# Kernel tuning notes

Measured on AMD Instinct MI355X. Metric: run time of the kernel, lower is better.

## Reference

```python
import jax, jax.numpy as jnp
import numpy as np

K = 256       # num states
M = 2         # markov order
D = 256       # lemb_size
V = 50000     # ntypes (vocab)
T = 512
B = 256
Kp1 = K + 1
EPS = 1e-5
INIT = 0.1


def _layernorm(h, g, b):
    mu = h.mean(-1, keepdims=True)
    var = ((h - mu) ** 2).mean(-1, keepdims=True)
    return (h - mu) / jnp.sqrt(var + EPS) * g + b


def setup_inputs() -> dict:
    key = jax.random.key(0)
    ks = jax.random.split(key, 12)
    u = lambda k, shp: jax.random.uniform(k, shp, jnp.float32, -INIT, INIT)
    return {
        "x": jax.random.randint(ks[0], (T, B), 0, V, dtype=jnp.int32),
        "z": jax.random.randint(ks[1], (T, B), 0, K, dtype=jnp.int32),
        "lembs": u(ks[2], (K, D)),
        "tlembs": u(ks[3], (Kp1, D)),
        "dec_W": u(ks[4], (V, D)),
        "dec_b": jnp.zeros((V,), jnp.float32),
        "em_W": u(ks[5], (D, D)),
        "em_bias": jnp.zeros((D,), jnp.float32),
        "em_g": jnp.ones((D,), jnp.float32),
        "em_beta": jnp.zeros((D,), jnp.float32),
        "td_W": u(ks[6], (K, M * D)),
        "td_b": jnp.zeros((K,), jnp.float32),
        "tm_W": u(ks[7], (M * D, M * D)),
        "tm_bias": jnp.zeros((M * D,), jnp.float32),
        "tn_g": jnp.ones((M * D,), jnp.float32),
        "tn_beta": jnp.zeros((M * D,), jnp.float32),
    }


def reference(x, z, lembs, tlembs, dec_W, dec_b, em_W, em_bias, em_g, em_beta,
              td_W, td_b, tm_W, tm_bias, tn_g, tn_beta):
    # --- emission distribution: K x V log-normalized ---
    h = _layernorm(lembs + jax.nn.relu(lembs @ em_W.T + em_bias), em_g, em_beta)
    emdist = jax.nn.log_softmax(h @ dec_W.T + dec_b, axis=1)  # (K, V)

    # --- transition distribution: (Kp1^M, K) log-normalized ---
    # cartesian product of label embeddings, row-major: row r <-> (i_0,...,i_{M-1})
    idx = jnp.indices((Kp1,) * M).reshape(M, -1)                 # (M, Kp1^M)
    cat = tlembs[idx].transpose(1, 0, 2).reshape(-1, M * D)      # (Kp1^M, M*D)
    th = _layernorm(cat + jax.nn.relu(cat @ tm_W.T + tm_bias), tn_g, tn_beta)
    transdist = jax.nn.log_softmax(th @ td_W.T + td_b, axis=1)   # (Kp1^M, K)

    # --- log_joint ---
    xlps = emdist.T[x]                                           # (T, B, K)
    emlps = jnp.take_along_axis(xlps, z[..., None].astype(jnp.int32), axis=2)[..., 0].sum(0)  # (B,)

    zpad = jnp.concatenate([jnp.full((M, B), K, dtype=z.dtype), z], axis=0)  # (T+M, B)
    win = jnp.stack([zpad[m:m + T] for m in range(M + 1)], 0)    # (M+1, T, B)
    lin = win[0]
    for m in range(1, M):
        lin = lin * Kp1 + win[m]                                 # row index into (Kp1^M, K)
    trans_lps = transdist[lin, win[M]]                           # (T, B)
    return emlps + trans_lps.sum(0)                              # (B,)
```

## Files before the change

kernel.cpp:

```cpp
#include <hip/hip_runtime.h>

#define Kst 256
#define Dd 256
#define Vv 50000
#define VPAD 50176
#define Tt 512
#define Bb 256
#define KP1 257
#define MD 512
#define NROWS (KP1*KP1)
#define EPSf 1e-5f

#define VB2 196
#define VB3 (VB2*4)

typedef __attribute__((ext_vector_type(8))) short short8;
typedef __attribute__((ext_vector_type(4))) float f32x4;
typedef __attribute__((ext_vector_type(4))) unsigned u32x4;
typedef __attribute__((ext_vector_type(2))) unsigned u32x2;

__device__ __forceinline__ unsigned short f2bf(float f) {
    unsigned u = __builtin_bit_cast(unsigned, f);
    unsigned r = (u + 0x7fffu + ((u >> 16) & 1u)) >> 16;
    return (unsigned short)r;
}
__device__ __forceinline__ float bf2f(unsigned short u) {
    return __builtin_bit_cast(float, ((unsigned)u) << 16);
}
__device__ __forceinline__ unsigned bfpack(float lo, float hi) {
    return __builtin_amdgcn_perm(__builtin_bit_cast(unsigned, hi),
                                 __builtin_bit_cast(unsigned, lo), 0x07060302u);
}
__device__ __forceinline__ unsigned f2bf2(float lo, float hi) {
    return (unsigned)f2bf(lo) | ((unsigned)f2bf(hi) << 16);
}

__global__ __launch_bounds__(256) void k_hP(
    const float* __restrict__ lembs, const float* __restrict__ em_W,
    const float* __restrict__ em_bias, const float* __restrict__ em_g,
    const float* __restrict__ em_beta, unsigned short* __restrict__ h_bf,
    const float* __restrict__ tlembs, const float* __restrict__ tm_W,
    float* __restrict__ P0, float* __restrict__ P1,
    const float* __restrict__ td_W, const float* __restrict__ tn_g,
    const float* __restrict__ tn_beta, const float* __restrict__ td_b,
    unsigned short* __restrict__ tdwg_bf, float* __restrict__ Gt,
    float* __restrict__ Bt, const float* __restrict__ dec_W,
    unsigned short* __restrict__ dwP)
{
    int bid = blockIdx.x;
    int tid = threadIdx.x, lane = tid & 63, wv = tid >> 6;
    int l15 = lane & 15, q = lane >> 4;

    if (bid >= 108) {
        int pb = bid - 108;
        int v = pb*8 + wv*2 + (lane >> 5);
        int l32 = lane & 31;
        int vr = v < Vv ? v : Vv-1;
        const float* src = dec_W + (size_t)vr*Dd + l32*8;
        float4 f0 = *(const float4*)(src);
        float4 f1 = *(const float4*)(src + 4);
        u32x4 pk;
        pk.x = bfpack(f0.x, f0.y);
        pk.y = bfpack(f0.z, f0.w);
        pk.z = bfpack(f1.x, f1.y);
        pk.w = bfpack(f1.z, f1.w);
        int ks = l32 >> 2, q2 = l32 & 3;
        int vb2 = v >> 8, vl = v & 255;
        int wvv = vl >> 6, ctv = vl & 3, l15v = (vl >> 2) & 15;
        *(short8*)(dwP + ((((size_t)vb2*8 + ks)*16 + wvv*4 + ctv)*64
                          + (q2*16 + l15v))*8) = __builtin_bit_cast(short8, pk);
        return;
    }

    if (bid >= 44) {
        int c = (bid - 44)*4 + wv;
        const float4* w4 = (const float4*)(td_W + (size_t)c*MD);
        const float4* g4 = (const float4*)tn_g;
        const float4* b4 = (const float4*)tn_beta;
        float sg = 0.f, sb = 0.f;
        short8 o;
        #pragma unroll
        for (int u = 0; u < 2; ++u) {
            int j4 = lane*2 + u;
            float4 w = w4[j4], g = g4[j4], bt = b4[j4];
            sg += w.x*g.x + w.y*g.y + w.z*g.z + w.w*g.w;
            sb += w.x*bt.x + w.y*bt.y + w.z*bt.z + w.w*bt.w;
            o[u*4+0] = (short)f2bf(w.x*g.x);
            o[u*4+1] = (short)f2bf(w.y*g.y);
            o[u*4+2] = (short)f2bf(w.z*g.z);
            o[u*4+3] = (short)f2bf(w.w*g.w);
        }
        {
            int wvv = c >> 6, l15v = (c >> 2) & 15, ctv = c & 3;
            int ksv = lane >> 2, qv = lane & 3;
            *(short8*)(tdwg_bf +
                ((((size_t)wvv*16 + ksv)*4 + ctv)*64 + (qv*16 + l15v))*8) = o;
        }
        #pragma unroll
        for (int dd = 32; dd > 0; dd >>= 1) {
            sg += __shfl_xor(sg, dd);
            sb += __shfl_xor(sb, dd);
        }
        if (lane == 0) { Gt[c] = sg; Bt[c] = sb + td_b[c]; }
        return;
    }

    __shared__ short ta[32][264];
    __shared__ float lsep[4][32][2];
    __shared__ float musig[32][2];

    int job, r0, cb, koff, BK;
    const float* Arow; const float* Brow;
    if (bid < 8) {
        job = 0; r0 = bid*32; cb = 0; koff = 0; BK = Dd;
        Arow = lembs; Brow = em_W;
    } else {
        int b2 = bid - 8;
        int half = b2 / 18;
        int b3 = b2 % 18;
        job = 1 + half;
        r0 = (b3 >> 1) * 32;
        cb = (b3 & 1) * 256;
        koff = half * 256; BK = MD;
        Arow = tlembs; Brow = tm_W;
    }

    {
        int row = tid >> 3, seg = (tid & 7) * 32;
        int r = r0 + row;
        if (r > 256) r = 256;
        const float4* s4 = (const float4*)(Arow + (size_t)r*Dd + seg);
        #pragma unroll
        for (int u = 0; u < 4; ++u) {
            float4 f0 = s4[u*2], f1 = s4[u*2+1];
            u32x4 pk;
            pk.x = bfpack(f0.x, f0.y);
            pk.y = bfpack(f0.z, f0.w);
            pk.z = bfpack(f1.x, f1.y);
            pk.w = bfpack(f1.z, f1.w);
            *(short8*)&ta[row][seg + u*8] = __builtin_bit_cast(short8, pk);
        }
    }
    __syncthreads();

    const float* bptr[4];
    #pragma unroll
    for (int ct = 0; ct < 4; ++ct) {
        int j = cb + wv*64 + ct*16 + l15;
        bptr[ct] = Brow + (size_t)j*BK + koff + q*8;
    }
    f32x4 acc[2][4];
    #pragma unroll
    for (int rt = 0; rt < 2; ++rt)
        #pragma unroll
        for (int ct = 0; ct < 4; ++ct)
            acc[rt][ct] = (f32x4){0.f,0.f,0.f,0.f};
    for (int ks = 0; ks < 8; ++ks) {
        short8 a0 = *(const short8*)&ta[ 0 + l15][ks*32 + q*8];
        short8 a1 = *(const short8*)&ta[16 + l15][ks*32 + q*8];
        short8 b[4];
        #pragma unroll
        for (int ct = 0; ct < 4; ++ct) {
            float4 f0 = *(const float4*)(bptr[ct] + ks*32);
            float4 f1 = *(const float4*)(bptr[ct] + ks*32 + 4);
            u32x4 pk;
            pk.x = bfpack(f0.x, f0.y);
            pk.y = bfpack(f0.z, f0.w);
            pk.z = bfpack(f1.x, f1.y);
            pk.w = bfpack(f1.z, f1.w);
            b[ct] = __builtin_bit_cast(short8, pk);
        }
        #pragma unroll
        for (int ct = 0; ct < 4; ++ct) {
            acc[0][ct] = __builtin_amdgcn_mfma_f32_16x16x32_bf16(a0, b[ct], acc[0][ct], 0,0,0);
            acc[1][ct] = __builtin_amdgcn_mfma_f32_16x16x32_bf16(a1, b[ct], acc[1][ct], 0,0,0);
        }
    }

    if (job != 0) {
        float* Pd = (job == 1) ? P0 : P1;
        #pragma unroll
        for (int rt = 0; rt < 2; ++rt) {
            #pragma unroll
            for (int reg = 0; reg < 4; ++reg) {
                int r = r0 + rt*16 + q*4 + reg;
                if (r < KP1) {
                    float* dst = Pd + (size_t)r*MD + cb + wv*64;
                    #pragma unroll
                    for (int ct = 0; ct < 4; ++ct)
                        dst[ct*16 + l15] = acc[rt][ct][reg];
                }
            }
        }
        return;
    }

    float bias_c[4];
    #pragma unroll
    for (int ct = 0; ct < 4; ++ct)
        bias_c[ct] = em_bias[wv*64 + ct*16 + l15];
    #pragma unroll
    for (int rt = 0; rt < 2; ++rt) {
        #pragma unroll
        for (int reg = 0; reg < 4; ++reg) {
            int r = r0 + rt*16 + q*4 + reg;
            #pragma unroll
            for (int ct = 0; ct < 4; ++ct) {
                float lv = lembs[(size_t)r*Dd + wv*64 + ct*16 + l15];
                acc[rt][ct][reg] = lv + fmaxf(acc[rt][ct][reg] + bias_c[ct], 0.f);
            }
        }
    }
    #pragma unroll
    for (int rt = 0; rt < 2; ++rt) {
        #pragma unroll
        for (int reg = 0; reg < 4; ++reg) {
            float s  = ((acc[rt][0][reg] + acc[rt][1][reg]) + (acc[rt][2][reg] + acc[rt][3][reg]));
            float ss = ((acc[rt][0][reg]*acc[rt][0][reg] + acc[rt][1][reg]*acc[rt][1][reg])
                      + (acc[rt][2][reg]*acc[rt][2][reg] + acc[rt][3][reg]*acc[rt][3][reg]));
            s  += __shfl_xor(s, 1);  ss += __shfl_xor(ss, 1);
            s  += __shfl_xor(s, 2);  ss += __shfl_xor(ss, 2);
            s  += __shfl_xor(s, 4);  ss += __shfl_xor(ss, 4);
            s  += __shfl_xor(s, 8);  ss += __shfl_xor(ss, 8);
            if (l15 == 0) {
                int rw = rt*16 + q*4 + reg;
                lsep[wv][rw][0] = s;
                lsep[wv][rw][1] = ss;
            }
        }
    }
    __syncthreads();
    if (tid < 32) {
        float s  = (lsep[0][tid][0] + lsep[1][tid][0]) + (lsep[2][tid][0] + lsep[3][tid][0]);
        float ss = (lsep[0][tid][1] + lsep[1][tid][1]) + (lsep[2][tid][1] + lsep[3][tid][1]);
        float mu = s * (1.f/Dd);
        musig[tid][0] = mu;
        musig[tid][1] = rsqrtf(ss*(1.f/Dd) - mu*mu + EPSf);
    }
    __syncthreads();
    float gl[4], bl[4];
    #pragma unroll
    for (int ct = 0; ct < 4; ++ct) {
        gl[ct] = em_g[wv*64 + ct*16 + l15];
        bl[ct] = em_beta[wv*64 + ct*16 + l15];
    }
    #pragma unroll
    for (int rt = 0; rt < 2; ++rt) {
        #pragma unroll
        for (int reg = 0; reg < 4; ++reg) {
            int rw = rt*16 + q*4 + reg;
            int r = r0 + rw;
            float mu = musig[rw][0], rs = musig[rw][1];
            unsigned short* dst = h_bf + (size_t)r*Dd + wv*64;
            #pragma unroll
            for (int ct = 0; ct < 4; ++ct)
                dst[ct*16 + l15] = f2bf((acc[rt][ct][reg] - mu)*rs*gl[ct] + bl[ct]);
        }
    }
}

__global__ __launch_bounds__(256) void k_em_mfma7(
    const unsigned short* __restrict__ dwP, const float* __restrict__ dec_b,
    const unsigned short* __restrict__ h_bf, float* __restrict__ part,
    unsigned short* __restrict__ E2)
{
    int kg = blockIdx.x, vb = blockIdx.y;
    int tid = threadIdx.x, lane = tid & 63, wv = tid >> 6;
    int l15 = lane & 15, q = lane >> 4;
    __shared__ short hs[64][264];

    {
        int row = tid >> 2, c0 = (tid & 3) * 64;
        const short8* src = (const short8*)(h_bf + (size_t)(kg*64 + row)*Dd + c0);
        #pragma unroll
        for (int u = 0; u < 8; ++u)
            *(short8*)&hs[row][c0 + u*8] = src[u];
    }
    __syncthreads();

    f32x4 acc[4][4];
    #pragma unroll
    for (int mt = 0; mt < 4; ++mt)
        #pragma unroll
        for (int ct = 0; ct < 4; ++ct)
            acc[mt][ct] = (f32x4){0.f,0.f,0.f,0.f};

    const short8* bb8 = (const short8*)dwP + ((size_t)vb*8*16 + wv*4)*64 + lane;
    short8 Bf[3][4];
    #define LDB_EM(slot, kk) { \
        Bf[slot][0] = bb8[((kk)*16 + 0)*64]; \
        Bf[slot][1] = bb8[((kk)*16 + 1)*64]; \
        Bf[slot][2] = bb8[((kk)*16 + 2)*64]; \
        Bf[slot][3] = bb8[((kk)*16 + 3)*64]; }
    LDB_EM(0, 0)
    LDB_EM(1, 1)
    #pragma unroll
    for (int ks = 0; ks < 8; ++ks) {
        if (ks < 6) LDB_EM((ks+2)%3, ks+2)
        short8 a[4];
        #pragma unroll
        for (int mt = 0; mt < 4; ++mt)
            a[mt] = *(const short8*)&hs[mt*16 + l15][ks*32 + q*8];
        #pragma unroll
        for (int mt = 0; mt < 4; ++mt)
            #pragma unroll
            for (int ct = 0; ct < 4; ++ct)
                acc[mt][ct] = __builtin_amdgcn_mfma_f32_16x16x32_bf16(a[mt], Bf[ks%3][ct], acc[mt][ct], 0,0,0);
    }
    #undef LDB_EM

    int vcol[4]; bool vok[4];
    #pragma unroll
    for (int ct = 0; ct < 4; ++ct) {
        int v = vb*256 + wv*64 + l15*4 + ct;
        vok[ct] = (v < Vv);
        vcol[ct] = v < Vv ? v : Vv-1;
    }
    #pragma unroll
    for (int ct = 0; ct < 4; ++ct) {
        if (vok[ct]) {
            float db = dec_b[vcol[ct]];
            #pragma unroll
            for (int mt = 0; mt < 4; ++mt)
                #pragma unroll
                for (int reg = 0; reg < 4; ++reg)
                    acc[mt][ct][reg] += db;
        } else {
            #pragma unroll
            for (int mt = 0; mt < 4; ++mt)
                #pragma unroll
                for (int reg = 0; reg < 4; ++reg)
                    acc[mt][ct][reg] = -1e30f;
        }
    }
    #pragma unroll
    for (int mt = 0; mt < 4; ++mt) {
        #pragma unroll
        for (int reg = 0; reg < 4; ++reg) {
            int k = kg*64 + mt*16 + q*4 + reg;
            u32x2 p;
            p.x = f2bf2(acc[mt][0][reg], acc[mt][1][reg]);
            p.y = f2bf2(acc[mt][2][reg], acc[mt][3][reg]);
            *(u32x2*)(E2 + (size_t)k*VPAD + vb*256 + wv*64 + l15*4) = p;
        }
    }
    #pragma unroll
    for (int mt = 0; mt < 4; ++mt) {
        #pragma unroll
        for (int reg = 0; reg < 4; ++reg) {
            float m = fmaxf(fmaxf(acc[mt][0][reg], acc[mt][1][reg]),
                            fmaxf(acc[mt][2][reg], acc[mt][3][reg]));
            m = fmaxf(m, __shfl_xor(m, 1));
            m = fmaxf(m, __shfl_xor(m, 2));
            m = fmaxf(m, __shfl_xor(m, 4));
            m = fmaxf(m, __shfl_xor(m, 8));
            float s = __expf(acc[mt][0][reg] - m) + __expf(acc[mt][1][reg] - m)
                    + __expf(acc[mt][2][reg] - m) + __expf(acc[mt][3][reg] - m);
            s += __shfl_xor(s, 1);
            s += __shfl_xor(s, 2);
            s += __shfl_xor(s, 4);
            s += __shfl_xor(s, 8);
            if (l15 == 0) {
                int k = kg*64 + mt*16 + q*4 + reg;
                part[((size_t)k*VB3 + vb*4 + wv)*2]     = m;
                part[((size_t)k*VB3 + vb*4 + wv)*2 + 1] = s;
            }
        }
    }
}

__global__ __launch_bounds__(64) void k_em_comb3(
    const float* __restrict__ part, float* __restrict__ lse_em)
{
    int k = blockIdx.x, lane = threadIdx.x;
    float m = -1e30f, s = 0.f;
    for (int vb = lane; vb < VB3; vb += 64) {
        float m2 = part[((size_t)k*VB3+vb)*2], s2 = part[((size_t)k*VB3+vb)*2+1];
        if (m2 > m) { s = s*__expf(m - m2) + s2; m = m2; }
        else          s += s2*__expf(m2 - m);
    }
    #pragma unroll
    for (int d = 1; d < 64; d <<= 1) {
        float mo = __shfl_xor(m, d), so = __shfl_xor(s, d);
        float mn = fmaxf(m, mo);
        s = s*__expf(m - mn) + so*__expf(mo - mn);
        m = mn;
    }
    if (lane == 0) lse_em[k] = m + logf(s);
}

__global__ __launch_bounds__(256, 4) void k_trans11(
    const float* __restrict__ tlembs, const float* __restrict__ P0,
    const float* __restrict__ P1, const float* __restrict__ tm_bias,
    const short* __restrict__ tdwg_bf, const float* __restrict__ Gt,
    const float* __restrict__ Bt, float* __restrict__ lse_t,
    unsigned short* __restrict__ Td)
{
    __shared__ short th[32][520];
    __shared__ float musig[32][2];
    __shared__ float lsep[4][32][2];
    int tid = threadIdx.x, lane = tid & 63, wv = tid >> 6;
    int l15 = lane & 15, q = lane >> 4;
    int r0 = blockIdx.x * 32;

    {
        const float4* bias0 = (const float4*)tm_bias;
        const float4* bias1 = (const float4*)(tm_bias + 256);
        float4 c0 = bias0[lane], c1 = bias1[lane];
        int i0a[8], i1a[8];
        #pragma unroll
        for (int i = 0; i < 8; ++i) {
            int r = r0 + wv*8 + i; if (r >= NROWS) r = NROWS - 1;
            i0a[i] = r / KP1; i1a[i] = r - i0a[i]*KP1;
        }
        float4 a0 = ((const float4*)(P0 + (size_t)i0a[0]*MD))[lane];
        float4 b0 = ((const float4*)(P1 + (size_t)i1a[0]*MD))[lane];
        float4 t0 = ((const float4*)(tlembs + (size_t)i0a[0]*Dd))[lane];
        float4 a1 = ((const float4*)(P0 + (size_t)i0a[0]*MD + 256))[lane];
        float4 b1 = ((const float4*)(P1 + (size_t)i1a[0]*MD + 256))[lane];
        float4 t1 = ((const float4*)(tlembs + (size_t)i1a[0]*Dd))[lane];
        #pragma unroll
        for (int i = 0; i < 8; ++i) {
            float4 na0, nb0, nt0, na1, nb1, nt1;
            if (i < 7) {
                na0 = ((const float4*)(P0 + (size_t)i0a[i+1]*MD))[lane];
                nb0 = ((const float4*)(P1 + (size_t)i1a[i+1]*MD))[lane];
                nt0 = ((const float4*)(tlembs + (size_t)i0a[i+1]*Dd))[lane];
                na1 = ((const float4*)(P0 + (size_t)i0a[i+1]*MD + 256))[lane];
                nb1 = ((const float4*)(P1 + (size_t)i1a[i+1]*MD + 256))[lane];
                nt1 = ((const float4*)(tlembs + (size_t)i1a[i+1]*Dd))[lane];
            }
            int row = wv*8 + i;
            float v0 = t0.x + fmaxf(a0.x+b0.x+c0.x, 0.f);
            float v1 = t0.y + fmaxf(a0.y+b0.y+c0.y, 0.f);
            float v2 = t0.z + fmaxf(a0.z+b0.z+c0.z, 0.f);
            float v3 = t0.w + fmaxf(a0.w+b0.w+c0.w, 0.f);
            float v4 = t1.x + fmaxf(a1.x+b1.x+c1.x, 0.f);
            float v5 = t1.y + fmaxf(a1.y+b1.y+c1.y, 0.f);
            float v6 = t1.z + fmaxf(a1.z+b1.z+c1.z, 0.f);
            float v7 = t1.w + fmaxf(a1.w+b1.w+c1.w, 0.f);
            u32x2 p0; p0.x = bfpack(v0, v1); p0.y = bfpack(v2, v3);
            u32x2 p1; p1.x = bfpack(v4, v5); p1.y = bfpack(v6, v7);
            *(u32x2*)&th[row][lane*4]       = p0;
            *(u32x2*)&th[row][256 + lane*4] = p1;
            float s  = ((v0+v1)+(v2+v3)) + ((v4+v5)+(v6+v7));
            float ss = ((v0*v0+v1*v1)+(v2*v2+v3*v3)) + ((v4*v4+v5*v5)+(v6*v6+v7*v7));
            #pragma unroll
            for (int d = 1; d < 64; d <<= 1) {
                s  += __shfl_xor(s, d);
                ss += __shfl_xor(ss, d);
            }
            if (lane == 0) {
                float mu = s * (1.f/MD);
                musig[row][0] = mu;
                musig[row][1] = rsqrtf(ss*(1.f/MD) - mu*mu + EPSf);
            }
            a0 = na0; b0 = nb0; t0 = nt0; a1 = na1; b1 = nb1; t1 = nt1;
        }
    }
    __syncthreads();

    f32x4 acc[2][4];
    #pragma unroll
    for (int rt = 0; rt < 2; ++rt)
        #pragma unroll
        for (int ct = 0; ct < 4; ++ct)
            acc[rt][ct] = (f32x4){0.f, 0.f, 0.f, 0.f};
    const short* bb = tdwg_bf + (size_t)wv*32768 + (size_t)lane*8;
    short8 Bf[3][4];
    #define LDB_TR(slot, kk) { const short* nxt = bb + (size_t)(kk)*2048; \
        Bf[slot][0] = *(const short8*)(nxt); \
        Bf[slot][1] = *(const short8*)(nxt + 512); \
        Bf[slot][2] = *(const short8*)(nxt + 1024); \
        Bf[slot][3] = *(const short8*)(nxt + 1536); }
    LDB_TR(0, 0)
    LDB_TR(1, 1)
    #pragma unroll
    for (int ks = 0; ks < 16; ++ks) {
        if (ks < 14) LDB_TR((ks+2)%3, ks+2)
        int ko = ks*32 + q*8;
        short8 a0 = *(const short8*)&th[ 0 + l15][ko];
        short8 a1 = *(const short8*)&th[16 + l15][ko];
        acc[0][0] = __builtin_amdgcn_mfma_f32_16x16x32_bf16(a0, Bf[ks%3][0], acc[0][0], 0,0,0);
        acc[1][0] = __builtin_amdgcn_mfma_f32_16x16x32_bf16(a1, Bf[ks%3][0], acc[1][0], 0,0,0);
        acc[0][1] = __builtin_amdgcn_mfma_f32_16x16x32_bf16(a0, Bf[ks%3][1], acc[0][1], 0,0,0);
        acc[1][1] = __builtin_amdgcn_mfma_f32_16x16x32_bf16(a1, Bf[ks%3][1], acc[1][1], 0,0,0);
        acc[0][2] = __builtin_amdgcn_mfma_f32_16x16x32_bf16(a0, Bf[ks%3][2], acc[0][2], 0,0,0);
        acc[1][2] = __builtin_amdgcn_mfma_f32_16x16x32_bf16(a1, Bf[ks%3][2], acc[1][2], 0,0,0);
        acc[0][3] = __builtin_amdgcn_mfma_f32_16x16x32_bf16(a0, Bf[ks%3][3], acc[0][3], 0,0,0);
        acc[1][3] = __builtin_amdgcn_mfma_f32_16x16x32_bf16(a1, Bf[ks%3][3], acc[1][3], 0,0,0);
    }
    #undef LDB_TR

    float4 Gc = *(const float4*)(Gt + wv*64 + l15*4);
    float4 Bc = *(const float4*)(Bt + wv*64 + l15*4);
    #pragma unroll
    for (int rt = 0; rt < 2; ++rt) {
        #pragma unroll
        for (int reg = 0; reg < 4; ++reg) {
            int rw = rt*16 + q*4 + reg;
            float mu = musig[rw][0], rs = musig[rw][1];
            float e0 = rs*(acc[rt][0][reg] - mu*Gc.x) + Bc.x;
            float e1 = rs*(acc[rt][1][reg] - mu*Gc.y) + Bc.y;
            float e2 = rs*(acc[rt][2][reg] - mu*Gc.z) + Bc.z;
            float e3 = rs*(acc[rt][3][reg] - mu*Gc.w) + Bc.w;
            long r = (long)r0 + rw;
            if (r < NROWS) {
                u32x2 p;
                p.x = f2bf2(e0, e1);
                p.y = f2bf2(e2, e3);
                *(u32x2*)(Td + (size_t)r*Kst + wv*64 + l15*4) = p;
            }
            float m = fmaxf(fmaxf(e0, e1), fmaxf(e2, e3));
            m = fmaxf(m, __shfl_xor(m, 1));
            m = fmaxf(m, __shfl_xor(m, 2));
            m = fmaxf(m, __shfl_xor(m, 4));
            m = fmaxf(m, __shfl_xor(m, 8));
            float s = __expf(e0 - m) + __expf(e1 - m) + __expf(e2 - m) + __expf(e3 - m);
            s += __shfl_xor(s, 1);
            s += __shfl_xor(s, 2);
            s += __shfl_xor(s, 4);
            s += __shfl_xor(s, 8);
            if (l15 == 0) {
                lsep[wv][rw][0] = m;
                lsep[wv][rw][1] = s;
            }
        }
    }
    __syncthreads();
    if (tid < 32) {
        int r = r0 + tid;
        if (r < NROWS) {
            float m0 = lsep[0][tid][0], m1 = lsep[1][tid][0];
            float m2 = lsep[2][tid][0], m3 = lsep[3][tid][0];
            float mg = fmaxf(fmaxf(m0, m1), fmaxf(m2, m3));
            float s = lsep[0][tid][1]*__expf(m0-mg) + lsep[1][tid][1]*__expf(m1-mg)
                    + lsep[2][tid][1]*__expf(m2-mg) + lsep[3][tid][1]*__expf(m3-mg);
            lse_t[r] = mg + logf(s);
        }
    }
}

#define GT_CH 2
__global__ __launch_bounds__(256) void k_gather3(
    const int* __restrict__ x, const int* __restrict__ z,
    const unsigned short* __restrict__ E2, const float* __restrict__ lse_em,
    const unsigned short* __restrict__ Td, const float* __restrict__ lse_t,
    float* __restrict__ out)
{
    int b = threadIdx.x;
    int t0 = blockIdx.x * GT_CH;
    float accv = 0.f;
    #pragma unroll
    for (int u = 0; u < GT_CH; ++u) {
        int t = t0 + u;
        int zc = z[t*Bb + b];
        int xv = x[t*Bb + b];
        int i0 = (t >= 2) ? z[(t-2)*Bb + b] : Kst;
        int i1 = (t >= 1) ? z[(t-1)*Bb + b] : Kst;
        int lin = i0*KP1 + i1;
        accv += bf2f(E2[(size_t)zc*VPAD + xv]) - lse_em[zc]
              + bf2f(Td[(size_t)lin*Kst + zc]) - lse_t[lin];
    }
    atomicAdd(&out[b], accv);
}

extern "C" void kernel_launch(void* const* d_in, const int* in_sizes, int n_in,
                              void* d_out, int out_size, void* d_ws, size_t ws_size,
                              hipStream_t stream)
{
    const int*   x       = (const int*)  d_in[0];
    const int*   z       = (const int*)  d_in[1];
    const float* lembs   = (const float*)d_in[2];
    const float* tlembs  = (const float*)d_in[3];
    const float* dec_W   = (const float*)d_in[4];
    const float* dec_b   = (const float*)d_in[5];
    const float* em_W    = (const float*)d_in[6];
    const float* em_bias = (const float*)d_in[7];
    const float* em_g    = (const float*)d_in[8];
    const float* em_beta = (const float*)d_in[9];
    const float* td_W    = (const float*)d_in[10];
    const float* td_b    = (const float*)d_in[11];
    const float* tm_W    = (const float*)d_in[12];
    const float* tm_bias = (const float*)d_in[13];
    const float* tn_g    = (const float*)d_in[14];
    const float* tn_beta = (const float*)d_in[15];
    float* out = (float*)d_out;

    float* ws     = (float*)d_ws;
    float* P0     = ws;
    float* P1     = P0 + 131584;
    float* lse_em = P1 + 131584;
    float* part   = lse_em + 256;
    float* lse_t  = part + 401408;
    float* Gt     = lse_t + 66052;
    float* Bt     = Gt + 256;
    unsigned short* tdwg_bf = (unsigned short*)(Bt + 256);
    unsigned short* h_bf   = tdwg_bf + 131072;
    unsigned short* E2     = h_bf + 65536;
    unsigned short* Td     = E2 + (size_t)Kst*VPAD;
    unsigned short* dwP    = Td + (size_t)NROWS*Kst;

    hipMemsetAsync(out, 0, Bb*sizeof(float), stream);
    k_hP<<<108 + VPAD/8, 256, 0, stream>>>(lembs, em_W, em_bias, em_g, em_beta, h_bf,
                                           tlembs, tm_W, P0, P1,
                                           td_W, tn_g, tn_beta, td_b, tdwg_bf, Gt, Bt,
                                           dec_W, dwP);
    k_em_mfma7<<<dim3(4, VB2), 256, 0, stream>>>(dwP, dec_b, h_bf, part, E2);
    k_em_comb3<<<Kst, 64, 0, stream>>>(part, lse_em);
    k_trans11<<<(NROWS + 31)/32, 256, 0, stream>>>(tlembs, P0, P1, tm_bias,
                                                   (const short*)tdwg_bf, Gt, Bt,
                                                   lse_t, Td);
    k_gather3<<<Tt/GT_CH, 256, 0, stream>>>(x, z, E2, lse_em, Td, lse_t, out);
}
```

Baseline: 235.4 us.

## Merge emission GEMM and transition kernel into one launch with XCD-aware mapping

Result: faster. 204.4 us (-13.2%).

```diff
diff --git a/kernel.cpp b/kernel.cpp
--- a/kernel.cpp
+++ b/kernel.cpp
@@ -13,6 +13,7 @@
 
 #define VB2 196
 #define VB3 (VB2*4)
+#define EMB 800
 
 typedef __attribute__((ext_vector_type(8))) short short8;
 typedef __attribute__((ext_vector_type(4))) float f32x4;
@@ -53,22 +54,29 @@
 
     if (bid >= 108) {
         int pb = bid - 108;
-        int v = pb*8 + wv*2 + (lane >> 5);
-        int l32 = lane & 31;
-        int vr = v < Vv ? v : Vv-1;
-        const float* src = dec_W + (size_t)vr*Dd + l32*8;
-        float4 f0 = *(const float4*)(src);
-        float4 f1 = *(const float4*)(src + 4);
-        u32x4 pk;
-        pk.x = bfpack(f0.x, f0.y);
-        pk.y = bfpack(f0.z, f0.w);
-        pk.z = bfpack(f1.x, f1.y);
-        pk.w = bfpack(f1.z, f1.w);
-        int ks = l32 >> 2, q2 = l32 & 3;
-        int vb2 = v >> 8, vl = v & 255;
-        int wvv = vl >> 6, ctv = vl & 3, l15v = (vl >> 2) & 15;
-        *(short8*)(dwP + ((((size_t)vb2*8 + ks)*16 + wvv*4 + ctv)*64
-                          + (q2*16 + l15v))*8) = __builtin_bit_cast(short8, pk);
+        int vb2 = pb >> 1, sub = pb & 1;
+        #pragma unroll 2
+        for (int j = 0; j < 8; ++j) {
+            int E0 = sub*4096 + wv*1024 + j*128 + lane*2;
+            #pragma unroll
+            for (int b = 0; b < 2; ++b) {
+                int E = E0 + b;
+                int ks = E >> 10, fi = (E >> 6) & 15, le = E & 63;
+                int q2 = le >> 4, lv = le & 15;
+                int v = ((fi >> 2) << 6) + lv*4 + (fi & 3);
+                int row = vb2*256 + v;
+                if (row > Vv-1) row = Vv-1;
+                const float* src = dec_W + (size_t)row*Dd + ks*32 + q2*8;
+                float4 f0 = *(const float4*)(src);
+                float4 f1 = *(const float4*)(src + 4);
+                u32x4 pk;
+                pk.x = bfpack(f0.x, f0.y);
+                pk.y = bfpack(f0.z, f0.w);
+                pk.z = bfpack(f1.x, f1.y);
+                pk.w = bfpack(f1.z, f1.w);
+                *(short8*)(dwP + ((size_t)vb2*8192 + E)*8) = __builtin_bit_cast(short8, pk);
+            }
+        }
         return;
     }
 
@@ -259,149 +267,138 @@
     }
 }
 
-__global__ __launch_bounds__(256) void k_em_mfma7(
+union SMemU {
+    struct { short hs[64][264]; } em;
+    struct { short th[32][520]; float musig[32][2]; float lsep[4][32][2]; } tr;
+};
+
+__global__ __launch_bounds__(256, 4) void k_emtrans(
     const unsigned short* __restrict__ dwP, const float* __restrict__ dec_b,
     const unsigned short* __restrict__ h_bf, float* __restrict__ part,
-    unsigned short* __restrict__ E2)
-{
-    int kg = blockIdx.x, vb = blockIdx.y;
-    int tid = threadIdx.x, lane = tid & 63, wv = tid >> 6;
-    int l15 = lane & 15, q = lane >> 4;
-    __shared__ short hs[64][264];
-
-    {
-        int row = tid >> 2, c0 = (tid & 3) * 64;
-        const short8* src = (const short8*)(h_bf + (size_t)(kg*64 + row)*Dd + c0);
-        #pragma unroll
-        for (int u = 0; u < 8; ++u)
-            *(short8*)&hs[row][c0 + u*8] = src[u];
-    }
-    __syncthreads();
-
-    f32x4 acc[4][4];
-    #pragma unroll
-    for (int mt = 0; mt < 4; ++mt)
-        #pragma unroll
-        for (int ct = 0; ct < 4; ++ct)
-            acc[mt][ct] = (f32x4){0.f,0.f,0.f,0.f};
-
-    const short8* bb8 = (const short8*)dwP + ((size_t)vb*8*16 + wv*4)*64 + lane;
-    short8 Bf[3][4];
-    #define LDB_EM(slot, kk) { \
-        Bf[slot][0] = bb8[((kk)*16 + 0)*64]; \
-        Bf[slot][1] = bb8[((kk)*16 + 1)*64]; \
-        Bf[slot][2] = bb8[((kk)*16 + 2)*64]; \
-        Bf[slot][3] = bb8[((kk)*16 + 3)*64]; }
-    LDB_EM(0, 0)
-    LDB_EM(1, 1)
-    #pragma unroll
-    for (int ks = 0; ks < 8; ++ks) {
-        if (ks < 6) LDB_EM((ks+2)%3, ks+2)
-        short8 a[4];
-        #pragma unroll
-        for (int mt = 0; mt < 4; ++mt)
-            a[mt] = *(const short8*)&hs[mt*16 + l15][ks*32 + q*8];
-        #pragma unroll
-        for (int mt = 0; mt < 4; ++mt)
-            #pragma unroll
-            for (int ct = 0; ct < 4; ++ct)
-                acc[mt][ct] = __builtin_amdgcn_mfma_f32_16x16x32_bf16(a[mt], Bf[ks%3][ct], acc[mt][ct], 0,0,0);
-    }
-    #undef LDB_EM
-
-    int vcol[4]; bool vok[4];
-    #pragma unroll
-    for (int ct = 0; ct < 4; ++ct) {
-        int v = vb*256 + wv*64 + l15*4 + ct;
-        vok[ct] = (v < Vv);
-        vcol[ct] = v < Vv ? v : Vv-1;
-    }
-    #pragma unroll
-    for (int ct = 0; ct < 4; ++ct) {
-        if (vok[ct]) {
-            float db = dec_b[vcol[ct]];
-            #pragma unroll
-            for (int mt = 0; mt < 4; ++mt)
-                #pragma unroll
-                for (int reg = 0; reg < 4; ++reg)
-                    acc[mt][ct][reg] += db;
-        } else {
-            #pragma unroll
-            for (int mt = 0; mt < 4; ++mt)
-                #pragma unroll
-                for (int reg = 0; reg < 4; ++reg)
-                    acc[mt][ct][reg] = -1e30f;
-        }
-    }
-    #pragma unroll
-    for (int mt = 0; mt < 4; ++mt) {
-        #pragma unroll
-        for (int reg = 0; reg < 4; ++reg) {
-            int k = kg*64 + mt*16 + q*4 + reg;
-            u32x2 p;
-            p.x = f2bf2(acc[mt][0][reg], acc[mt][1][reg]);
-            p.y = f2bf2(acc[mt][2][reg], acc[mt][3][reg]);
-            *(u32x2*)(E2 + (size_t)k*VPAD + vb*256 + wv*64 + l15*4) = p;
-        }
-    }
-    #pragma unroll
-    for (int mt = 0; mt < 4; ++mt) {
-        #pragma unroll
-        for (int reg = 0; reg < 4; ++reg) {
-            float m = fmaxf(fmaxf(acc[mt][0][reg], acc[mt][1][reg]),
-                            fmaxf(acc[mt][2][reg], acc[mt][3][reg]));
-            m = fmaxf(m, __shfl_xor(m, 1));
-            m = fmaxf(m, __shfl_xor(m, 2));
-            m = fmaxf(m, __shfl_xor(m, 4));
-            m = fmaxf(m, __shfl_xor(m, 8));
-            float s = __expf(acc[mt][0][reg] - m) + __expf(acc[mt][1][reg] - m)
-                    + __expf(acc[mt][2][reg] - m) + __expf(acc[mt][3][reg] - m);
-            s += __shfl_xor(s, 1);
-            s += __shfl_xor(s, 2);
-            s += __shfl_xor(s, 4);
-            s += __shfl_xor(s, 8);
-            if (l15 == 0) {
-                int k = kg*64 + mt*16 + q*4 + reg;
-                part[((size_t)k*VB3 + vb*4 + wv)*2]     = m;
-                part[((size_t)k*VB3 + vb*4 + wv)*2 + 1] = s;
-            }
-        }
-    }
-}
-
-__global__ __launch_bounds__(64) void k_em_comb3(
-    const float* __restrict__ part, float* __restrict__ lse_em)
-{
-    int k = blockIdx.x, lane = threadIdx.x;
-    float m = -1e30f, s = 0.f;
-    for (int vb = lane; vb < VB3; vb += 64) {
-        float m2 = part[((size_t)k*VB3+vb)*2], s2 = part[((size_t)k*VB3+vb)*2+1];
-        if (m2 > m) { s = s*__expf(m - m2) + s2; m = m2; }
-        else          s += s2*__expf(m2 - m);
-    }
-    #pragma unroll
-    for (int d = 1; d < 64; d <<= 1) {
-        float mo = __shfl_xor(m, d), so = __shfl_xor(s, d);
-        float mn = fmaxf(m, mo);
-        s = s*__expf(m - mn) + so*__expf(mo - mn);
-        m = mn;
-    }
-    if (lane == 0) lse_em[k] = m + logf(s);
-}
-
-__global__ __launch_bounds__(256, 4) void k_trans11(
+    unsigned short* __restrict__ E2,
     const float* __restrict__ tlembs, const float* __restrict__ P0,
     const float* __restrict__ P1, const float* __restrict__ tm_bias,
     const short* __restrict__ tdwg_bf, const float* __restrict__ Gt,
     const float* __restrict__ Bt, float* __restrict__ lse_t,
     unsigned short* __restrict__ Td)
 {
-    __shared__ short th[32][520];
-    __shared__ float musig[32][2];
-    __shared__ float lsep[4][32][2];
+    __shared__ SMemU sm;
+    int bid = blockIdx.x;
     int tid = threadIdx.x, lane = tid & 63, wv = tid >> 6;
     int l15 = lane & 15, q = lane >> 4;
-    int r0 = blockIdx.x * 32;
+
+    if (bid < EMB) {
+        int xcd = bid & 7, slot = bid >> 3;
+        int grp = slot >> 2, kg = slot & 3;
+        int vb = grp*8 + xcd;
+        if (vb >= VB2) return;
+        short (*hs)[264] = sm.em.hs;
+
+        {
+            int row = tid >> 2, c0 = (tid & 3) * 64;
+            const short8* src = (const short8*)(h_bf + (size_t)(kg*64 + row)*Dd + c0);
+            #pragma unroll
+            for (int u = 0; u < 8; ++u)
+                *(short8*)&hs[row][c0 + u*8] = src[u];
+        }
+        __syncthreads();
+
+        f32x4 acc[4][4];
+        #pragma unroll
+        for (int mt = 0; mt < 4; ++mt)
+            #pragma unroll
+            for (int ct = 0; ct < 4; ++ct)
+                acc[mt][ct] = (f32x4){0.f,0.f,0.f,0.f};
+
+        const short8* bb8 = (const short8*)dwP + ((size_t)vb*8*16 + wv*4)*64 + lane;
+        short8 Bf[3][4];
+        #define LDB_EM(slot_, kk) { \
+            Bf[slot_][0] = bb8[((kk)*16 + 0)*64]; \
+            Bf[slot_][1] = bb8[((kk)*16 + 1)*64]; \
+            Bf[slot_][2] = bb8[((kk)*16 + 2)*64]; \
+            Bf[slot_][3] = bb8[((kk)*16 + 3)*64]; }
+        LDB_EM(0, 0)
+        LDB_EM(1, 1)
+        #pragma unroll
+        for (int ks = 0; ks < 8; ++ks) {
+            if (ks < 6) LDB_EM((ks+2)%3, ks+2)
+            short8 a[4];
+            #pragma unroll
+            for (int mt = 0; mt < 4; ++mt)
+                a[mt] = *(const short8*)&hs[mt*16 + l15][ks*32 + q*8];
+            #pragma unroll
+            for (int mt = 0; mt < 4; ++mt)
+                #pragma unroll
+                for (int ct = 0; ct < 4; ++ct)
+                    acc[mt][ct] = __builtin_amdgcn_mfma_f32_16x16x32_bf16(a[mt], Bf[ks%3][ct], acc[mt][ct], 0,0,0);
+        }
+        #undef LDB_EM
+
+        int vcol[4]; bool vok[4];
+        #pragma unroll
+        for (int ct = 0; ct < 4; ++ct) {
+            int v = vb*256 + wv*64 + l15*4 + ct;
+            vok[ct] = (v < Vv);
+            vcol[ct] = v < Vv ? v : Vv-1;
+        }
+        #pragma unroll
+        for (int ct = 0; ct < 4; ++ct) {
+            if (vok[ct]) {
+                float db = dec_b[vcol[ct]];
+                #pragma unroll
+                for (int mt = 0; mt < 4; ++mt)
+                    #pragma unroll
+                    for (int reg = 0; reg < 4; ++reg)
+                        acc[mt][ct][reg] += db;
+            } else {
+                #pragma unroll
+                for (int mt = 0; mt < 4; ++mt)
+                    #pragma unroll
+                    for (int reg = 0; reg < 4; ++reg)
+                        acc[mt][ct][reg] = -1e30f;
+            }
+        }
+        #pragma unroll
+        for (int mt = 0; mt < 4; ++mt) {
+            #pragma unroll
+            for (int reg = 0; reg < 4; ++reg) {
+                int k = kg*64 + mt*16 + q*4 + reg;
+                u32x2 p;
+                p.x = f2bf2(acc[mt][0][reg], acc[mt][1][reg]);
+                p.y = f2bf2(acc[mt][2][reg], acc[mt][3][reg]);
+                *(u32x2*)(E2 + (size_t)k*VPAD + vb*256 + wv*64 + l15*4) = p;
+            }
+        }
+        #pragma unroll
+        for (int mt = 0; mt < 4; ++mt) {
+            #pragma unroll
+            for (int reg = 0; reg < 4; ++reg) {
+                float m = fmaxf(fmaxf(acc[mt][0][reg], acc[mt][1][reg]),
+                                fmaxf(acc[mt][2][reg], acc[mt][3][reg]));
+                m = fmaxf(m, __shfl_xor(m, 1));
+                m = fmaxf(m, __shfl_xor(m, 2));
+                m = fmaxf(m, __shfl_xor(m, 4));
+                m = fmaxf(m, __shfl_xor(m, 8));
+                float s = __expf(acc[mt][0][reg] - m) + __expf(acc[mt][1][reg] - m)
+                        + __expf(acc[mt][2][reg] - m) + __expf(acc[mt][3][reg] - m);
+                s += __shfl_xor(s, 1);
+                s += __shfl_xor(s, 2);
+                s += __shfl_xor(s, 4);
+                s += __shfl_xor(s, 8);
+                if (l15 == 0) {
+                    int k = kg*64 + mt*16 + q*4 + reg;
+                    part[((size_t)k*VB3 + vb*4 + wv)*2]     = m;
+                    part[((size_t)k*VB3 + vb*4 + wv)*2 + 1] = s;
+                }
+            }
+        }
+        return;
+    }
+
+    short (*th)[520]   = sm.tr.th;
+    float (*musig)[2]  = sm.tr.musig;
+    float (*lsep)[32][2] = sm.tr.lsep;
+    int r0 = (bid - EMB) * 32;
 
     {
         const float4* bias0 = (const float4*)tm_bias;
@@ -413,50 +410,57 @@
             int r = r0 + wv*8 + i; if (r >= NROWS) r = NROWS - 1;
             i0a[i] = r / KP1; i1a[i] = r - i0a[i]*KP1;
         }
-        float4 a0 = ((const float4*)(P0 + (size_t)i0a[0]*MD))[lane];
-        float4 b0 = ((const float4*)(P1 + (size_t)i1a[0]*MD))[lane];
-        float4 t0 = ((const float4*)(tlembs + (size_t)i0a[0]*Dd))[lane];
-        float4 a1 = ((const float4*)(P0 + (size_t)i0a[0]*MD + 256))[lane];
-        float4 b1 = ((const float4*)(P1 + (size_t)i1a[0]*MD + 256))[lane];
-        float4 t1 = ((const float4*)(tlembs + (size_t)i1a[0]*Dd))[lane];
-        #pragma unroll
-        for (int i = 0; i < 8; ++i) {
-            float4 na0, nb0, nt0, na1, nb1, nt1;
-            if (i < 7) {
-                na0 = ((const float4*)(P0 + (size_t)i0a[i+1]*MD))[lane];
-                nb0 = ((const float4*)(P1 + (size_t)i1a[i+1]*MD))[lane];
-                nt0 = ((const float4*)(tlembs + (size_t)i0a[i+1]*Dd))[lane];
-                na1 = ((const float4*)(P0 + (size_t)i0a[i+1]*MD + 256))[lane];
-                nb1 = ((const float4*)(P1 + (size_t)i1a[i+1]*MD + 256))[lane];
-                nt1 = ((const float4*)(tlembs + (size_t)i1a[i+1]*Dd))[lane];
-            }
-            int row = wv*8 + i;
-            float v0 = t0.x + fmaxf(a0.x+b0.x+c0.x, 0.f);
-            float v1 = t0.y + fmaxf(a0.y+b0.y+c0.y, 0.f);
-            float v2 = t0.z + fmaxf(a0.z+b0.z+c0.z, 0.f);
-            float v3 = t0.w + fmaxf(a0.w+b0.w+c0.w, 0.f);
-            float v4 = t1.x + fmaxf(a1.x+b1.x+c1.x, 0.f);
-            float v5 = t1.y + fmaxf(a1.y+b1.y+c1.y, 0.f);
-            float v6 = t1.z + fmaxf(a1.z+b1.z+c1.z, 0.f);
-            float v7 = t1.w + fmaxf(a1.w+b1.w+c1.w, 0.f);
-            u32x2 p0; p0.x = bfpack(v0, v1); p0.y = bfpack(v2, v3);
-            u32x2 p1; p1.x = bfpack(v4, v5); p1.y = bfpack(v6, v7);
-            *(u32x2*)&th[row][lane*4]       = p0;
-            *(u32x2*)&th[row][256 + lane*4] = p1;
-            float s  = ((v0+v1)+(v2+v3)) + ((v4+v5)+(v6+v7));
-            float ss = ((v0*v0+v1*v1)+(v2*v2+v3*v3)) + ((v4*v4+v5*v5)+(v6*v6+v7*v7));
-            #pragma unroll
-            for (int d = 1; d < 64; d <<= 1) {
-                s  += __shfl_xor(s, d);
-                ss += __shfl_xor(ss, d);
-            }
-            if (lane == 0) {
-                float mu = s * (1.f/MD);
-                musig[row][0] = mu;
-                musig[row][1] = rsqrtf(ss*(1.f/MD) - mu*mu + EPSf);
-            }
-            a0 = na0; b0 = nb0; t0 = nt0; a1 = na1; b1 = nb1; t1 = nt1;
-        }
+        #define ROWBODY(i, A0, B0, T0, A1, B1, T1) { \
+            int row = wv*8 + (i); \
+            float v0 = (T0).x + fmaxf((A0).x+(B0).x+c0.x, 0.f); \
+            float v1 = (T0).y + fmaxf((A0).y+(B0).y+c0.y, 0.f); \
+            float v2 = (T0).z + fmaxf((A0).z+(B0).z+c0.z, 0.f); \
+            float v3 = (T0).w + fmaxf((A0).w+(B0).w+c0.w, 0.f); \
+            float v4 = (T1).x + fmaxf((A1).x+(B1).x+c1.x, 0.f); \
+            float v5 = (T1).y + fmaxf((A1).y+(B1).y+c1.y, 0.f); \
+            float v6 = (T1).z + fmaxf((A1).z+(B1).z+c1.z, 0.f); \
+            float v7 = (T1).w + fmaxf((A1).w+(B1).w+c1.w, 0.f); \
+            u32x2 p0; p0.x = bfpack(v0, v1); p0.y = bfpack(v2, v3); \
+            u32x2 p1; p1.x = bfpack(v4, v5); p1.y = bfpack(v6, v7); \
+            *(u32x2*)&th[row][lane*4]       = p0; \
+            *(u32x2*)&th[row][256 + lane*4] = p1; \
+            float s  = ((v0+v1)+(v2+v3)) + ((v4+v5)+(v6+v7)); \
+            float ss = ((v0*v0+v1*v1)+(v2*v2+v3*v3)) + ((v4*v4+v5*v5)+(v6*v6+v7*v7)); \
+            _Pragma("unroll") \
+            for (int d = 1; d < 64; d <<= 1) { \
+                s  += __shfl_xor(s, d); \
+                ss += __shfl_xor(ss, d); \
+            } \
+            if (lane == 0) { \
+                float mu = s * (1.f/MD); \
+                musig[row][0] = mu; \
+                musig[row][1] = rsqrtf(ss*(1.f/MD) - mu*mu + EPSf); \
+            } }
+
+        if (i0a[0] == i0a[7]) {
+            float4 A0 = ((const float4*)(P0 + (size_t)i0a[0]*MD))[lane];
+            float4 A1 = ((const float4*)(P0 + (size_t)i0a[0]*MD + 256))[lane];
+            float4 T0 = ((const float4*)(tlembs + (size_t)i0a[0]*Dd))[lane];
+            #pragma unroll
+            for (int i = 0; i < 8; ++i) {
+                float4 b0 = ((const float4*)(P1 + (size_t)i1a[i]*MD))[lane];
+                float4 b1 = ((const float4*)(P1 + (size_t)i1a[i]*MD + 256))[lane];
+                float4 t1 = ((const float4*)(tlembs + (size_t)i1a[i]*Dd))[lane];
+                ROWBODY(i, A0, b0, T0, A1, b1, t1)
+            }
+        } else {
+            #pragma unroll
+            for (int i = 0; i < 8; ++i) {
+                float4 A0 = ((const float4*)(P0 + (size_t)i0a[i]*MD))[lane];
+                float4 A1 = ((const float4*)(P0 + (size_t)i0a[i]*MD + 256))[lane];
+                float4 T0 = ((const float4*)(tlembs + (size_t)i0a[i]*Dd))[lane];
+                float4 b0 = ((const float4*)(P1 + (size_t)i1a[i]*MD))[lane];
+                float4 b1 = ((const float4*)(P1 + (size_t)i1a[i]*MD + 256))[lane];
+                float4 t1 = ((const float4*)(tlembs + (size_t)i1a[i]*Dd))[lane];
+                ROWBODY(i, A0, b0, T0, A1, b1, t1)
+            }
+        }
+        #undef ROWBODY
     }
     __syncthreads();
 
@@ -468,11 +472,11 @@
             acc[rt][ct] = (f32x4){0.f, 0.f, 0.f, 0.f};
     const short* bb = tdwg_bf + (size_t)wv*32768 + (size_t)lane*8;
     short8 Bf[3][4];
-    #define LDB_TR(slot, kk) { const short* nxt = bb + (size_t)(kk)*2048; \
-        Bf[slot][0] = *(const short8*)(nxt); \
-        Bf[slot][1] = *(const short8*)(nxt + 512); \
-        Bf[slot][2] = *(const short8*)(nxt + 1024); \
-        Bf[slot][3] = *(const short8*)(nxt + 1536); }
+    #define LDB_TR(slot_, kk) { const short* nxt = bb + (size_t)(kk)*2048; \
+        Bf[slot_][0] = *(const short8*)(nxt); \
+        Bf[slot_][1] = *(const short8*)(nxt + 512); \
+        Bf[slot_][2] = *(const short8*)(nxt + 1024); \
+        Bf[slot_][3] = *(const short8*)(nxt + 1536); }
     LDB_TR(0, 0)
     LDB_TR(1, 1)
     #pragma unroll
@@ -539,6 +543,26 @@
             lse_t[r] = mg + logf(s);
         }
     }
+}
+
+__global__ __launch_bounds__(64) void k_em_comb3(
+    const float* __restrict__ part, float* __restrict__ lse_em)
+{
+    int k = blockIdx.x, lane = threadIdx.x;
+    float m = -1e30f, s = 0.f;
+    for (int vb = lane; vb < VB3; vb += 64) {
+        float m2 = part[((size_t)k*VB3+vb)*2], s2 = part[((size_t)k*VB3+vb)*2+1];
+        if (m2 > m) { s = s*__expf(m - m2) + s2; m = m2; }
+        else          s += s2*__expf(m2 - m);
+    }
+    #pragma unroll
+    for (int d = 1; d < 64; d <<= 1) {
+        float mo = __shfl_xor(m, d), so = __shfl_xor(s, d);
+        float mn = fmaxf(m, mo);
+        s = s*__expf(m - mn) + so*__expf(mo - mn);
+        m = mn;
+    }
+    if (lane == 0) lse_em[k] = m + logf(s);
 }
 
 #define GT_CH 2
@@ -602,14 +626,13 @@
     unsigned short* dwP    = Td + (size_t)NROWS*Kst;
 
     hipMemsetAsync(out, 0, Bb*sizeof(float), stream);
-    k_hP<<<108 + VPAD/8, 256, 0, stream>>>(lembs, em_W, em_bias, em_g, em_beta, h_bf,
-                                           tlembs, tm_W, P0, P1,
-                                           td_W, tn_g, tn_beta, td_b, tdwg_bf, Gt, Bt,
-                                           dec_W, dwP);
-    k_em_mfma7<<<dim3(4, VB2), 256, 0, stream>>>(dwP, dec_b, h_bf, part, E2);
+    k_hP<<<108 + 392, 256, 0, stream>>>(lembs, em_W, em_bias, em_g, em_beta, h_bf,
+                                        tlembs, tm_W, P0, P1,
+                                        td_W, tn_g, tn_beta, td_b, tdwg_bf, Gt, Bt,
+                                        dec_W, dwP);
+    k_emtrans<<<EMB + (NROWS + 31)/32, 256, 0, stream>>>(
+        dwP, dec_b, h_bf, part, E2,
+        tlembs, P0, P1, tm_bias, (const short*)tdwg_bf, Gt, Bt, lse_t, Td);
     k_em_comb3<<<Kst, 64, 0, stream>>>(part, lse_em);
-    k_trans11<<<(NROWS + 31)/32, 256, 0, stream>>>(tlembs, P0, P1, tm_bias,
-                                                   (const short*)tdwg_bf, Gt, Bt,
-                                                   lse_t, Td);
     k_gather3<<<Tt/GT_CH, 256, 0, stream>>>(x, z, E2, lse_em, Td, lse_t, out);
 }
```
